# Kernel tuning notes

Measured on AMD Instinct MI355X. Metric: run time of the kernel, lower is better.

## Reference

```python
import jax, jax.numpy as jnp
import numpy as np

N_HEAD = 16
HEAD_SIZE = 64

def setup_inputs() -> dict:
    key = jax.random.key(0)
    ks = jax.random.split(key, 5)
    B, T, C = 2, 2048, 1024
    s = 0.02
    return {
        "x": jax.random.normal(ks[0], (B, T, C), dtype=jnp.float32),
        "We": jax.random.normal(ks[1], (3 * C, C), dtype=jnp.float32) * s,
        "be": jax.random.normal(ks[2], (3 * C,), dtype=jnp.float32) * s,
        "Wp": jax.random.normal(ks[3], (C, C), dtype=jnp.float32) * s,
        "bp": jax.random.normal(ks[4], (C,), dtype=jnp.float32) * s,
    }

def reference(x, We, be, Wp, bp):
    B, T, C = x.shape
    H, D = N_HEAD, HEAD_SIZE
    qkv = x @ We.T + be                      # [B,T,3C]
    q, k, v = jnp.split(qkv, 3, axis=-1)
    # [B,H,T,D]
    q = q.reshape(B, T, H, D).transpose(0, 2, 1, 3)
    k = k.reshape(B, T, H, D).transpose(0, 2, 1, 3)
    v = v.reshape(B, T, H, D).transpose(0, 2, 1, 3)
    scale = 1.0 / jnp.sqrt(jnp.asarray(D, dtype=x.dtype))
    att = jnp.einsum('bhqd,bhkd->bhqk', q, k) * scale
    causal = jnp.tril(jnp.ones((T, T), dtype=bool))
    att = jnp.where(causal, att, -jnp.inf)
    att = jax.nn.softmax(att, axis=-1)
    y = jnp.einsum('bhqk,bhkd->bhqd', att, v)   # [B,H,T,D]
    y = y.transpose(0, 2, 1, 3).reshape(B, T, C)
    return y @ Wp.T + bp
```

## Files before the change

### kernel.cpp

```cpp
#include <hip/hip_runtime.h>
#include <hip/hip_bf16.h>
#include <stdint.h>
#include <stddef.h>

typedef short s8v __attribute__((ext_vector_type(8)));
typedef float f4v __attribute__((ext_vector_type(4)));

__device__ inline float b2f(short s) {
    union { unsigned u; float f; } x;
    x.u = ((unsigned)(unsigned short)s) << 16;
    return x.f;
}
__device__ inline short f2b(float f) {
    union { float f; unsigned u; } x;
    x.f = f;
    unsigned r = x.u + 0x7FFF + ((x.u >> 16) & 1);
    return (short)(r >> 16);
}

__device__ __forceinline__ void gl16(const short* g, short* l) {
    __builtin_amdgcn_global_load_lds(
        (const __attribute__((address_space(1))) void*)g,
        (__attribute__((address_space(3))) void*)l,
        16, 0, 0);
}

__global__ void detect_dtype(const unsigned* __restrict__ x, int* __restrict__ flag)
{
    int hit = 0;
    for (int i = threadIdx.x; i < 1024; i += 64) {
        unsigned lo = x[i] & 0xFFFFu;
        unsigned e = (lo >> 7) & 0xFFu;
        if (e >= 0x8Au) hit = 1;
    }
    unsigned long long any = __ballot(hit != 0);
    if (threadIdx.x == 0) *flag = (any != 0ull) ? 1 : 0;
}

__global__ __launch_bounds__(256) void convert_bf16(
    const void* s0, short* d0, size_t c0,
    const void* s1, short* d1, size_t c1,
    const void* s2, short* d2, size_t c2,
    const void* s3, short* d3, size_t c3,
    const void* s4, short* d4, size_t c4,
    const int* __restrict__ flagp)
{
    const bool f32 = (*flagp != 0);
    const void* srcs[5] = {s0, s1, s2, s3, s4};
    short* dsts[5] = {d0, d1, d2, d3, d4};
    size_t cnts[5] = {c0, c1, c2, c3, c4};
    size_t total = c0 + c1 + c2 + c3 + c4;
    size_t stride = (size_t)gridDim.x * blockDim.x;
    for (size_t c = (size_t)blockIdx.x * blockDim.x + threadIdx.x; c < total; c += stride) {
        size_t r = c; int s = 0;
        while (r >= cnts[s]) { r -= cnts[s]; s++; }
        short* d = dsts[s] + r * 8;
        if (f32) {
            const float* p = (const float*)srcs[s] + r * 8;
            f4v a = *(const f4v*)p;
            f4v b = *(const f4v*)(p + 4);
            s8v v;
            v[0] = f2b(a[0]); v[1] = f2b(a[1]); v[2] = f2b(a[2]); v[3] = f2b(a[3]);
            v[4] = f2b(b[0]); v[5] = f2b(b[1]); v[6] = f2b(b[2]); v[7] = f2b(b[3]);
            *(s8v*)d = v;
        } else {
            *(s8v*)d = *(const s8v*)((const short*)srcs[s] + r * 8);
        }
    }
}

#define BM 128
#define BN 128
#define BKK 64

template<int QKV>
__global__ __launch_bounds__(256) void gemm_bt_bias(
    const short* __restrict__ A,
    const short* __restrict__ B,
    const short* __restrict__ bias,
    void* __restrict__ C,
    short* __restrict__ vT,
    int M, int N, int K, int ldc,
    const int* __restrict__ flagp, int oDyn)
{
    const bool of32 = oDyn && (*flagp != 0);

    __shared__ __align__(16) short smem[QKV ? (128 * 136) : (BM + BN) * BKK];
    short* sA = smem;
    short* sB = smem + BM * BKK;

    const int tid  = threadIdx.x;
    const int lane = tid & 63;
    const int w    = tid >> 6;
    const int wm   = (w >> 1) * 64;
    const int wn   = (w & 1) * 64;
    const int quad = lane >> 4;
    const int l16  = lane & 15;

    const int m0 = blockIdx.y * BM;
    const int n0 = blockIdx.x * BN;

    f4v acc[4][4];
    const f4v vzero = {0.0f, 0.0f, 0.0f, 0.0f};
#pragma unroll
    for (int i = 0; i < 4; i++)
#pragma unroll
        for (int j = 0; j < 4; j++) acc[i][j] = vzero;

    for (int k0 = 0; k0 < K; k0 += BKK) {
        __syncthreads();
#pragma unroll
        for (int i = 0; i < 4; i++) {
            int c  = i * 256 + tid;
            int r  = c >> 3, kk = (c & 7) * 8;
            int cb = i * 256 + (tid & 192);
            gl16(A + (size_t)(m0 + r) * K + k0 + kk, sA + cb * 8);
            gl16(B + (size_t)(n0 + r) * K + k0 + kk, sB + cb * 8);
        }
        __syncthreads();
#pragma unroll
        for (int s = 0; s < 2; s++) {
            s8v af[4], bf[4];
#pragma unroll
            for (int t = 0; t < 4; t++)
                af[t] = *(const s8v*)(sA + (wm + t * 16 + l16) * BKK + s * 32 + quad * 8);
#pragma unroll
            for (int t = 0; t < 4; t++)
                bf[t] = *(const s8v*)(sB + (wn + t * 16 + l16) * BKK + s * 32 + quad * 8);
#pragma unroll
            for (int mt = 0; mt < 4; mt++)
#pragma unroll
                for (int nt = 0; nt < 4; nt++)
                    acc[mt][nt] = __builtin_amdgcn_mfma_f32_16x16x32_bf16(
                        af[mt], bf[nt], acc[mt][nt], 0, 0, 0);
        }
    }

    if (QKV && n0 >= 2048) {
        __syncthreads();
#pragma unroll
        for (int nt = 0; nt < 4; nt++) {
            int nl = wn + nt * 16 + l16;
            float bv = b2f(bias[n0 + nl]);
#pragma unroll
            for (int mt = 0; mt < 4; mt++)
#pragma unroll
                for (int r = 0; r < 4; r++) {
                    int ml = wm + mt * 16 + quad * 4 + r;
                    smem[nl * 136 + ml] = f2b(acc[mt][nt][r] + bv);
                }
        }
        __syncthreads();
        int nl = tid >> 1, half = tid & 1;
        int n = n0 + nl;
        int h = (n - 2048) >> 6, d = n & 63;
        int bq = m0 >> 11;
        short* dst = vT + (((size_t)(bq * 16 + h)) * 64 + d) * 2048 + (m0 & 2047) + half * 64;
        const short* src = smem + nl * 136 + half * 64;
#pragma unroll
        for (int j = 0; j < 8; j++)
            *(s8v*)(dst + j * 8) = *(const s8v*)(src + j * 8);
    } else {
#pragma unroll
        for (int nt = 0; nt < 4; nt++) {
            int n = n0 + wn + nt * 16 + l16;
            float bv = b2f(bias[n]);
#pragma unroll
            for (int mt = 0; mt < 4; mt++) {
#pragma unroll
                for (int r = 0; r < 4; r++) {
                    int m = m0 + wm + mt * 16 + quad * 4 + r;
                    float v = acc[mt][nt][r] + bv;
                    if (of32) ((float*)C)[(size_t)m * ldc + n] = v;
                    else      ((short*)C)[(size_t)m * ldc + n] = f2b(v);
                }
            }
        }
    }
}

#define LP 72

__global__ __launch_bounds__(256) void attn_flash(
    const short* __restrict__ qk,
    const short* __restrict__ vt,
    short* __restrict__ y)
{
    const int T = 2048, LDQ = 2048;
    __shared__ __align__(16) short sK[64 * LP];
    __shared__ __align__(16) short sVT[64 * LP];
    __shared__ __align__(16) short sP[4][16 * LP];

    const int tid  = threadIdx.x;
    const int lane = tid & 63;
    const int w    = tid >> 6;
    const int quad = lane >> 4;
    const int l16  = lane & 15;

    const int bx = blockIdx.x;
    const int qt = 31 - (bx >> 5);
    const int bh = bx & 31;
    const int b  = bh >> 4;
    const int h  = bh & 15;

    const size_t qkbase = (size_t)b * T * LDQ;
    const short* Kbase  = qk + qkbase + 1024 + h * 64;
    const short* Vbase  = vt + (size_t)bh * 64 * 2048;

    s8v qf[2];
    {
        int qrow = qt * 64 + w * 16 + l16;
        const short* qp = qk + qkbase + (size_t)qrow * LDQ + h * 64 + quad * 8;
        qf[0] = *(const s8v*)(qp);
        qf[1] = *(const s8v*)(qp + 32);
    }

    const f4v vzero = {0.0f, 0.0f, 0.0f, 0.0f};
    f4v o[4];
#pragma unroll
    for (int i = 0; i < 4; i++) o[i] = vzero;
    float lsum[4] = {0.0f, 0.0f, 0.0f, 0.0f};

    for (int kt = 0; kt <= qt; kt++) {
        __syncthreads();
#pragma unroll
        for (int i = 0; i < 2; i++) {
            int c = i * 256 + tid;
            int r = c >> 3, dd = (c & 7) * 8;
            s8v kv = *(const s8v*)(Kbase + (size_t)(kt * 64 + r) * LDQ + dd);
            s8v vv = *(const s8v*)(Vbase + (size_t)r * 2048 + kt * 64 + dd);
            *(s8v*)(sK  + r * LP + dd) = kv;
            *(s8v*)(sVT + r * LP + dd) = vv;
        }
        __syncthreads();

        f4v sacc[4];
#pragma unroll
        for (int nt = 0; nt < 4; nt++) {
            sacc[nt] = vzero;
            s8v kf0 = *(const s8v*)(sK + (nt * 16 + l16) * LP + quad * 8);
            s8v kf1 = *(const s8v*)(sK + (nt * 16 + l16) * LP + 32 + quad * 8);
            sacc[nt] = __builtin_amdgcn_mfma_f32_16x16x32_bf16(qf[0], kf0, sacc[nt], 0, 0, 0);
            sacc[nt] = __builtin_amdgcn_mfma_f32_16x16x32_bf16(qf[1], kf1, sacc[nt], 0, 0, 0);
        }

        short* pp = sP[w];
        const bool diag = (kt == qt);
#pragma unroll
        for (int nt = 0; nt < 4; nt++) {
#pragma unroll
            for (int r = 0; r < 4; r++) {
                float p = __expf(sacc[nt][r] * 0.125f);
                if (diag) {
                    int q = w * 16 + quad * 4 + r;
                    int k = nt * 16 + l16;
                    if (k > q) p = 0.0f;
                }
                lsum[r] += p;
                pp[(quad * 4 + r) * LP + nt * 16 + l16] = f2b(p);
            }
        }
        __syncthreads();

        s8v pf0 = *(const s8v*)(pp + l16 * LP + quad * 8);
        s8v pf1 = *(const s8v*)(pp + l16 * LP + 32 + quad * 8);
#pragma unroll
        for (int dt = 0; dt < 4; dt++) {
            s8v vf0 = *(const s8v*)(sVT + (dt * 16 + l16) * LP + quad * 8);
            s8v vf1 = *(const s8v*)(sVT + (dt * 16 + l16) * LP + 32 + quad * 8);
            o[dt] = __builtin_amdgcn_mfma_f32_16x16x32_bf16(pf0, vf0, o[dt], 0, 0, 0);
            o[dt] = __builtin_amdgcn_mfma_f32_16x16x32_bf16(pf1, vf1, o[dt], 0, 0, 0);
        }
    }

#pragma unroll
    for (int r = 0; r < 4; r++) {
        float s = lsum[r];
        s += __shfl_xor(s, 1, 64);
        s += __shfl_xor(s, 2, 64);
        s += __shfl_xor(s, 4, 64);
        s += __shfl_xor(s, 8, 64);
        lsum[r] = 1.0f / s;
    }
#pragma unroll
    for (int dt = 0; dt < 4; dt++)
#pragma unroll
        for (int r = 0; r < 4; r++) {
            int qrow = qt * 64 + w * 16 + quad * 4 + r;
            int d = dt * 16 + l16;
            y[((size_t)b * T + qrow) * 1024 + h * 64 + d] = f2b(o[dt][r] * lsum[r]);
        }
}

extern "C" void kernel_launch(void* const* d_in, const int* in_sizes, int n_in,
                              void* d_out, int out_size, void* d_ws, size_t ws_size,
                              hipStream_t stream)
{
    int*   flag = (int*)d_ws;
    short* qk   = (short*)((char*)d_ws + 16);
    short* vT   = qk  + (size_t)4096 * 2048;
    short* xb   = vT  + (size_t)32 * 64 * 2048;
    short* Web  = xb  + (size_t)4096 * 1024;
    short* Wpb  = Web + (size_t)3072 * 1024;
    short* beb  = Wpb + (size_t)1024 * 1024;
    short* bpb  = beb + 3072;
    short* y    = xb;

    detect_dtype<<<1, 64, 0, stream>>>((const unsigned*)d_in[0], flag);

    convert_bf16<<<dim3(4098), 256, 0, stream>>>(
        d_in[0], xb,  (size_t)4096 * 1024 / 8,
        d_in[1], Web, (size_t)3072 * 1024 / 8,
        d_in[2], beb, (size_t)3072 / 8,
        d_in[3], Wpb, (size_t)1024 * 1024 / 8,
        d_in[4], bpb, (size_t)1024 / 8,
        flag);

    gemm_bt_bias<1><<<dim3(3072 / BN, 4096 / BM), 256, 0, stream>>>(
        xb, Web, beb, qk, vT, 4096, 3072, 1024, 2048, flag, 0);

    attn_flash<<<dim3(1024), 256, 0, stream>>>(qk, vT, y);

    gemm_bt_bias<0><<<dim3(1024 / BN, 4096 / BM), 256, 0, stream>>>(
        y, Wpb, bpb, d_out, nullptr, 4096, 1024, 1024, 1024, flag, 1);
}
```

Baseline: 228.4 us.

## Split causal attention KV range across two blocks, combine, and shrink output GEMM tile

Attention work is split along the key dimension into two halves handled by separate blocks, which write unnormalized partial outputs and row sums; a new combine kernel adds them and normalizes. The output projection GEMM switches to a 64-wide N tile so it launches more blocks. The 1/sqrt(D) scale moves into the QKV GEMM epilogue, and the row sum accumulates the bf16-truncated probabilities. This adds a partial-buffer round trip and an extra launch in exchange for better load balance and occupancy across the GPU's compute units. Partials are stored in bf16, which may cost some precision.

After: 216.5 us. -5.2%, faster.

```diff
diff --git a/kernel.cpp b/kernel.cpp
--- a/kernel.cpp
+++ b/kernel.cpp
@@ -70,10 +70,9 @@
 }
 
 #define BM 128
-#define BN 128
 #define BKK 64
 
-template<int QKV>
+template<int QKV, int TBN>
 __global__ __launch_bounds__(256) void gemm_bt_bias(
     const short* __restrict__ A,
     const short* __restrict__ B,
@@ -84,8 +83,9 @@
     const int* __restrict__ flagp, int oDyn)
 {
     const bool of32 = oDyn && (*flagp != 0);
-
-    __shared__ __align__(16) short smem[QKV ? (128 * 136) : (BM + BN) * BKK];
+    const int NT = TBN / 32;
+
+    __shared__ __align__(16) short smem[QKV ? (128 * 136) : (BM + TBN) * BKK];
     short* sA = smem;
     short* sB = smem + BM * BKK;
 
@@ -93,19 +93,19 @@
     const int lane = tid & 63;
     const int w    = tid >> 6;
     const int wm   = (w >> 1) * 64;
-    const int wn   = (w & 1) * 64;
+    const int wn   = (w & 1) * (TBN / 2);
     const int quad = lane >> 4;
     const int l16  = lane & 15;
 
     const int m0 = blockIdx.y * BM;
-    const int n0 = blockIdx.x * BN;
-
-    f4v acc[4][4];
+    const int n0 = blockIdx.x * TBN;
+
+    f4v acc[4][NT];
     const f4v vzero = {0.0f, 0.0f, 0.0f, 0.0f};
 #pragma unroll
     for (int i = 0; i < 4; i++)
 #pragma unroll
-        for (int j = 0; j < 4; j++) acc[i][j] = vzero;
+        for (int j = 0; j < NT; j++) acc[i][j] = vzero;
 
     for (int k0 = 0; k0 < K; k0 += BKK) {
         __syncthreads();
@@ -115,22 +115,23 @@
             int r  = c >> 3, kk = (c & 7) * 8;
             int cb = i * 256 + (tid & 192);
             gl16(A + (size_t)(m0 + r) * K + k0 + kk, sA + cb * 8);
-            gl16(B + (size_t)(n0 + r) * K + k0 + kk, sB + cb * 8);
+            if (i < TBN / 32)
+                gl16(B + (size_t)(n0 + r) * K + k0 + kk, sB + cb * 8);
         }
         __syncthreads();
 #pragma unroll
         for (int s = 0; s < 2; s++) {
-            s8v af[4], bf[4];
+            s8v af[4], bf[NT];
 #pragma unroll
             for (int t = 0; t < 4; t++)
                 af[t] = *(const s8v*)(sA + (wm + t * 16 + l16) * BKK + s * 32 + quad * 8);
 #pragma unroll
-            for (int t = 0; t < 4; t++)
+            for (int t = 0; t < NT; t++)
                 bf[t] = *(const s8v*)(sB + (wn + t * 16 + l16) * BKK + s * 32 + quad * 8);
 #pragma unroll
             for (int mt = 0; mt < 4; mt++)
 #pragma unroll
-                for (int nt = 0; nt < 4; nt++)
+                for (int nt = 0; nt < NT; nt++)
                     acc[mt][nt] = __builtin_amdgcn_mfma_f32_16x16x32_bf16(
                         af[mt], bf[nt], acc[mt][nt], 0, 0, 0);
         }
@@ -139,7 +140,7 @@
     if (QKV && n0 >= 2048) {
         __syncthreads();
 #pragma unroll
-        for (int nt = 0; nt < 4; nt++) {
+        for (int nt = 0; nt < NT; nt++) {
             int nl = wn + nt * 16 + l16;
             float bv = b2f(bias[n0 + nl]);
 #pragma unroll
@@ -161,8 +162,9 @@
         for (int j = 0; j < 8; j++)
             *(s8v*)(dst + j * 8) = *(const s8v*)(src + j * 8);
     } else {
-#pragma unroll
-        for (int nt = 0; nt < 4; nt++) {
+        const float osc = (QKV && n0 < 1024) ? 0.125f : 1.0f;
+#pragma unroll
+        for (int nt = 0; nt < NT; nt++) {
             int n = n0 + wn + nt * 16 + l16;
             float bv = b2f(bias[n]);
 #pragma unroll
@@ -170,7 +172,7 @@
 #pragma unroll
                 for (int r = 0; r < 4; r++) {
                     int m = m0 + wm + mt * 16 + quad * 4 + r;
-                    float v = acc[mt][nt][r] + bv;
+                    float v = (acc[mt][nt][r] + bv) * osc;
                     if (of32) ((float*)C)[(size_t)m * ldc + n] = v;
                     else      ((short*)C)[(size_t)m * ldc + n] = f2b(v);
                 }
@@ -181,10 +183,13 @@
 
 #define LP 72
 
+template<int PARTS>
 __global__ __launch_bounds__(256) void attn_flash(
     const short* __restrict__ qk,
     const short* __restrict__ vt,
-    short* __restrict__ y)
+    short* __restrict__ y,
+    short* __restrict__ Opart,
+    float* __restrict__ Lpart)
 {
     const int T = 2048, LDQ = 2048;
     __shared__ __align__(16) short sK[64 * LP];
@@ -197,11 +202,36 @@
     const int quad = lane >> 4;
     const int l16  = lane & 15;
 
-    const int bx = blockIdx.x;
-    const int qt = 31 - (bx >> 5);
-    const int bh = bx & 31;
-    const int b  = bh >> 4;
-    const int h  = bh & 15;
+    int part, qt, bh, u;
+    if (PARTS == 2) {
+        part = blockIdx.x & 1;
+        int rest = blockIdx.x >> 1;
+        qt = 31 - (rest >> 5);
+        bh = rest & 31;
+        u  = bh * 32 + qt;
+    } else {
+        part = 0;
+        qt = 31 - (blockIdx.x >> 5);
+        bh = blockIdx.x & 31;
+        u  = 0;
+    }
+    const int b = bh >> 4;
+    const int h = bh & 15;
+
+    const int n    = qt + 1;
+    const int half = (n + 1) >> 1;
+    const int klo  = (PARTS == 2 && part) ? half : 0;
+    const int khi  = (PARTS == 2 && !part) ? half : n;
+
+    if (PARTS == 2 && klo >= khi) {
+        s8v z;
+#pragma unroll
+        for (int j = 0; j < 8; j++) z[j] = 0;
+        s8v* ob = (s8v*)(Opart + ((size_t)(part * 1024 + u)) * 4096);
+        for (int i = tid; i < 512; i += 256) ob[i] = z;
+        if (tid < 64) Lpart[(size_t)(part * 1024 + u) * 64 + tid] = 0.0f;
+        return;
+    }
 
     const size_t qkbase = (size_t)b * T * LDQ;
     const short* Kbase  = qk + qkbase + 1024 + h * 64;
@@ -221,7 +251,7 @@
     for (int i = 0; i < 4; i++) o[i] = vzero;
     float lsum[4] = {0.0f, 0.0f, 0.0f, 0.0f};
 
-    for (int kt = 0; kt <= qt; kt++) {
+    for (int kt = klo; kt < khi; kt++) {
         __syncthreads();
 #pragma unroll
         for (int i = 0; i < 2; i++) {
@@ -250,14 +280,17 @@
         for (int nt = 0; nt < 4; nt++) {
 #pragma unroll
             for (int r = 0; r < 4; r++) {
-                float p = __expf(sacc[nt][r] * 0.125f);
+                float p = __expf(sacc[nt][r]);
                 if (diag) {
                     int q = w * 16 + quad * 4 + r;
                     int k = nt * 16 + l16;
                     if (k > q) p = 0.0f;
                 }
-                lsum[r] += p;
-                pp[(quad * 4 + r) * LP + nt * 16 + l16] = f2b(p);
+                union { float f; unsigned u; } c; c.f = p;
+                short p16 = (short)(c.u >> 16);
+                c.u &= 0xFFFF0000u;
+                lsum[r] += c.f;
+                pp[(quad * 4 + r) * LP + nt * 16 + l16] = p16;
             }
         }
         __syncthreads();
@@ -280,31 +313,80 @@
         s += __shfl_xor(s, 2, 64);
         s += __shfl_xor(s, 4, 64);
         s += __shfl_xor(s, 8, 64);
-        lsum[r] = 1.0f / s;
-    }
-#pragma unroll
-    for (int dt = 0; dt < 4; dt++)
-#pragma unroll
-        for (int r = 0; r < 4; r++) {
-            int qrow = qt * 64 + w * 16 + quad * 4 + r;
-            int d = dt * 16 + l16;
-            y[((size_t)b * T + qrow) * 1024 + h * 64 + d] = f2b(o[dt][r] * lsum[r]);
-        }
+        lsum[r] = s;
+    }
+
+    if (PARTS == 2) {
+        short* ob = Opart + ((size_t)(part * 1024 + u)) * 4096;
+#pragma unroll
+        for (int dt = 0; dt < 4; dt++)
+#pragma unroll
+            for (int r = 0; r < 4; r++)
+                ob[(w * 16 + quad * 4 + r) * 64 + dt * 16 + l16] = f2b(o[dt][r]);
+        if (l16 == 0) {
+#pragma unroll
+            for (int r = 0; r < 4; r++)
+                Lpart[(size_t)(part * 1024 + u) * 64 + w * 16 + quad * 4 + r] = lsum[r];
+        }
+    } else {
+#pragma unroll
+        for (int r = 0; r < 4; r++) lsum[r] = 1.0f / lsum[r];
+#pragma unroll
+        for (int dt = 0; dt < 4; dt++)
+#pragma unroll
+            for (int r = 0; r < 4; r++) {
+                int qrow = qt * 64 + w * 16 + quad * 4 + r;
+                int d = dt * 16 + l16;
+                y[((size_t)b * T + qrow) * 1024 + h * 64 + d] = f2b(o[dt][r] * lsum[r]);
+            }
+    }
+}
+
+__global__ __launch_bounds__(256) void attn_combine(
+    const short* __restrict__ Opart,
+    const float* __restrict__ Lpart,
+    short* __restrict__ y)
+{
+    const int u  = blockIdx.x;
+    const int bh = u >> 5, qt = u & 31;
+    const int b = bh >> 4, h = bh & 15;
+    const int t = threadIdx.x;
+    const int q = t >> 2, dg = (t & 3) * 16;
+
+    float l = Lpart[(size_t)u * 64 + q] + Lpart[(size_t)(1024 + u) * 64 + q];
+    float rl = 1.0f / l;
+    const short* p0 = Opart + (size_t)u * 4096 + q * 64 + dg;
+    const short* p1 = Opart + (size_t)(1024 + u) * 4096 + q * 64 + dg;
+    short* yo = y + ((size_t)b * 2048 + qt * 64 + q) * 1024 + h * 64 + dg;
+#pragma unroll
+    for (int hv = 0; hv < 2; hv++) {
+        s8v a = *(const s8v*)(p0 + hv * 8);
+        s8v c = *(const s8v*)(p1 + hv * 8);
+        s8v r;
+#pragma unroll
+        for (int j = 0; j < 8; j++) r[j] = f2b((b2f(a[j]) + b2f(c[j])) * rl);
+        *(s8v*)(yo + hv * 8) = r;
+    }
 }
 
 extern "C" void kernel_launch(void* const* d_in, const int* in_sizes, int n_in,
                               void* d_out, int out_size, void* d_ws, size_t ws_size,
                               hipStream_t stream)
 {
-    int*   flag = (int*)d_ws;
-    short* qk   = (short*)((char*)d_ws + 16);
-    short* vT   = qk  + (size_t)4096 * 2048;
-    short* xb   = vT  + (size_t)32 * 64 * 2048;
-    short* Web  = xb  + (size_t)4096 * 1024;
-    short* Wpb  = Web + (size_t)3072 * 1024;
-    short* beb  = Wpb + (size_t)1024 * 1024;
-    short* bpb  = beb + 3072;
-    short* y    = xb;
+    char* p = (char*)d_ws;
+    int*   flag = (int*)p;                 p += 16;
+    short* qk   = (short*)p;               p += (size_t)4096 * 2048 * 2;
+    short* vT   = (short*)p;               p += (size_t)32 * 64 * 2048 * 2;
+    short* xb   = (short*)p;               p += (size_t)4096 * 1024 * 2;
+    short* Web  = (short*)p;               p += (size_t)3072 * 1024 * 2;
+    short* Wpb  = (short*)p;               p += (size_t)1024 * 1024 * 2;
+    short* beb  = (short*)p;               p += 3072 * 2;
+    short* bpb  = (short*)p;               p += 1024 * 2;
+    short* Opart = (short*)p;              p += (size_t)2 * 1024 * 4096 * 2;
+    float* Lpart = (float*)p;              p += (size_t)2 * 1024 * 64 * 4;
+    short* y = xb;
+    const size_t need = (size_t)(p - (char*)d_ws);
+    const bool split = (ws_size >= need);
 
     detect_dtype<<<1, 64, 0, stream>>>((const unsigned*)d_in[0], flag);
 
@@ -316,11 +398,16 @@
         d_in[4], bpb, (size_t)1024 / 8,
         flag);
 
-    gemm_bt_bias<1><<<dim3(3072 / BN, 4096 / BM), 256, 0, stream>>>(
+    gemm_bt_bias<1, 128><<<dim3(3072 / 128, 4096 / BM), 256, 0, stream>>>(
         xb, Web, beb, qk, vT, 4096, 3072, 1024, 2048, flag, 0);
 
-    attn_flash<<<dim3(1024), 256, 0, stream>>>(qk, vT, y);
-
-    gemm_bt_bias<0><<<dim3(1024 / BN, 4096 / BM), 256, 0, stream>>>(
+    if (split) {
+        attn_flash<2><<<dim3(2048), 256, 0, stream>>>(qk, vT, nullptr, Opart, Lpart);
+        attn_combine<<<dim3(1024), 256, 0, stream>>>(Opart, Lpart, y);
+    } else {
+        attn_flash<1><<<dim3(1024), 256, 0, stream>>>(qk, vT, y, nullptr, nullptr);
+    }
+
+    gemm_bt_bias<0, 64><<<dim3(1024 / 64, 4096 / BM), 256, 0, stream>>>(
         y, Wpb, bpb, d_out, nullptr, 4096, 1024, 1024, 1024, flag, 1);
 }
```
